# Optimization experiments

Hardware: AMD Instinct MI355X
Metric: run time of the kernel (lower is better)

## Reference

```python
import jax, jax.numpy as jnp
import numpy as np

N_NODES = 50000
N_EDGES = 400000
D_IN = 512
D_OUT = 512
MASK_RATE = 0.3


def setup_inputs() -> dict:
    key = jax.random.key(0)
    k1, k2, k3, k4, k5 = jax.random.split(key, 5)
    feat = jax.random.normal(k1, (N_NODES, D_IN), dtype=jnp.float32)
    # xavier_uniform for weight [in_feat, out_feat]
    limit = float(np.sqrt(6.0 / (D_IN + D_OUT)))
    weight = jax.random.uniform(k2, (D_IN, D_OUT), dtype=jnp.float32, minval=-limit, maxval=limit)
    edge_src = jax.random.randint(k3, (N_EDGES,), 0, N_NODES, dtype=jnp.int64 if jax.config.jax_enable_x64 else jnp.int32)
    edge_dst = jax.random.randint(k4, (N_EDGES,), 0, N_NODES, dtype=jnp.int64 if jax.config.jax_enable_x64 else jnp.int32)
    edge_val = jax.random.uniform(k5, (N_EDGES,), dtype=jnp.float32)
    # deterministic stand-in for torch.randperm(...)[:num_mask]
    perm = jax.random.permutation(jax.random.fold_in(key, 7), N_NODES)
    mask_idx = perm[: int(MASK_RATE * N_NODES)]
    return {
        "feat": feat,
        "weight": weight,
        "edge_val": edge_val,
        "edge_src": edge_src,
        "edge_dst": edge_dst,
        "mask_idx": mask_idx,
    }


def reference(feat, weight, edge_val, edge_src, edge_dst, mask_idx):
    # zero out masked node rows (encoding_mask_noise)
    out_x = feat.at[mask_idx].set(0.0)
    # dense transform: [N, D_in] @ [D_in, D_out]
    x = out_x @ weight
    # spmm(adj, x): for edge (src -> dst, val): out[dst] += val * x[src]
    msgs = edge_val[:, None] * x[edge_src]  # [E, D_out]
    out = jax.ops.segment_sum(msgs, edge_dst, num_segments=feat.shape[0])
    return out, mask_idx
```

## Files before the change

### kernel.cpp

```cpp
#include <hip/hip_runtime.h>

#define DD 512
#define SCAN_B 256
#define BM 128
#define BN 256
#define BK 32
#define NSTEP 16
typedef unsigned short u16;
typedef unsigned int u32;

typedef __attribute__((ext_vector_type(8))) __bf16 bf16v8;
typedef __attribute__((ext_vector_type(4))) float f32x4;

__device__ __forceinline__ u16 f2bf(float f) {
  u32 u = __builtin_bit_cast(u32, f);
  u32 r = (u + 0x7fffu + ((u >> 16) & 1u)) >> 16;
  return (u16)r;
}
__device__ __forceinline__ float bf2f(u32 h) {
  return __builtin_bit_cast(float, h << 16);
}
__device__ __forceinline__ u32 pk2(float a, float b) {
  return f2bf(a) | ((u32)f2bf(b) << 16);
}

typedef const __attribute__((address_space(1))) void* gptr_t;
typedef __attribute__((address_space(3))) void* lptr_t;
__device__ __forceinline__ void gload_lds16(const void* g, void* l) {
  __builtin_amdgcn_global_load_lds((gptr_t)g, (lptr_t)l, 16, 0, 0);
}

#define BAR_N(N)                                                        \
  do {                                                                  \
    __builtin_amdgcn_sched_barrier(0);                                  \
    asm volatile("s_waitcnt vmcnt(" #N ") lgkmcnt(0)\n\ts_barrier" ::: "memory"); \
  } while (0)

__global__ __launch_bounds__(256) void wconv_t(const float* __restrict__ W,
                                               u16* __restrict__ Wt) {
  __shared__ float sm[64][65];
  const int bx = blockIdx.x;
  const int by = blockIdx.y;
  const int t = threadIdx.x;
  const int r = t >> 6;
  const int c = t & 63;
#pragma unroll
  for (int i = 0; i < 64; i += 4)
    sm[i + r][c] = W[(size_t)(bx * 64 + i + r) * DD + by * 64 + c];
  __syncthreads();
#pragma unroll
  for (int i = 0; i < 64; i += 4) {
    const int n = by * 64 + i + r;
    const int k = bx * 64 + c;
    Wt[(size_t)n * DD + k] = f2bf(sm[c][i + r]);
  }
}

__global__ __launch_bounds__(512) void gemm_pipe(const float* __restrict__ A,
                                                 const u16* __restrict__ Bt,
                                                 u16* __restrict__ X, int M) {
  __shared__ __align__(16) u16 ldsA[2][BM * BK];
  __shared__ __align__(16) u16 ldsB[3][BN * BK];
  const int tid = threadIdx.x;
  const int lane = tid & 63;
  const int w = tid >> 6;
  const int wm = w >> 2;
  const int wn = w & 3;
  const int row0 = blockIdx.y * BM;
  const int colB = blockIdx.x * BN;
  const int lr = lane & 15;
  const int kg = lane >> 4;

  f32x4 acc[4][4] = {};

  const int arow = tid >> 2;
  const int agk = (tid & 3) ^ ((arow >> 1) & 3);
  int ar = row0 + arow;
  if (ar >= M) ar = M - 1;
  const float* gA = A + (size_t)ar * DD + agk * 8;
  const int laoff = tid * 8;

  const u16* gB[2];
  int lB[2];
#pragma unroll
  for (int q = 0; q < 2; ++q) {
    const int c = (w * 2 + q) * 64 + lane;
    const int col = c >> 2, kc = c & 3;
    const int gk = kc ^ ((col >> 1) & 3);
    gB[q] = Bt + (size_t)(colB + col) * DD + gk * 8;
    lB[q] = c * 8;
  }

  f32x4 rP[2][2];

#pragma unroll
  for (int q = 0; q < 2; ++q) gload_lds16(gB[q], &ldsB[0][lB[q]]);
#pragma unroll
  for (int q = 0; q < 2; ++q) gload_lds16(gB[q] + BK, &ldsB[1][lB[q]]);
  rP[0][0] = *(const f32x4*)(gA);
  rP[0][1] = *(const f32x4*)(gA + 4);
  rP[1][0] = *(const f32x4*)(gA + BK);
  rP[1][1] = *(const f32x4*)(gA + BK + 4);
  {
    uint4 pk;
    pk.x = pk2(rP[0][0].x, rP[0][0].y);
    pk.y = pk2(rP[0][0].z, rP[0][0].w);
    pk.z = pk2(rP[0][1].x, rP[0][1].y);
    pk.w = pk2(rP[0][1].z, rP[0][1].w);
    *(uint4*)&ldsA[0][laoff] = pk;
  }
  BAR_N(2);

#pragma unroll
  for (int t = 0; t < NSTEP; ++t) {
    if (t + 2 < NSTEP) {
#pragma unroll
      for (int q = 0; q < 2; ++q)
        gload_lds16(gB[q] + (t + 2) * BK, &ldsB[(t + 2) % 3][lB[q]]);
    }

    bf16v8 af[4], bfr[4];
#pragma unroll
    for (int m = 0; m < 4; ++m) {
      const int row = wm * 64 + m * 16 + lr;
      const int kc = kg ^ ((row >> 1) & 3);
      af[m] = *(const bf16v8*)&ldsA[t & 1][row * BK + kc * 8];
    }
#pragma unroll
    for (int n = 0; n < 4; ++n) {
      const int col = wn * 64 + n * 16 + lr;
      const int kc = kg ^ ((col >> 1) & 3);
      bfr[n] = *(const bf16v8*)&ldsB[t % 3][col * BK + kc * 8];
    }
#pragma unroll
    for (int m = 0; m < 4; ++m)
#pragma unroll
      for (int n = 0; n < 4; ++n)
        acc[m][n] = __builtin_amdgcn_mfma_f32_16x16x32_bf16(af[m], bfr[n], acc[m][n], 0, 0, 0);

    if (t + 1 < NSTEP) {
      uint4 pk;
      pk.x = pk2(rP[(t + 1) & 1][0].x, rP[(t + 1) & 1][0].y);
      pk.y = pk2(rP[(t + 1) & 1][0].z, rP[(t + 1) & 1][0].w);
      pk.z = pk2(rP[(t + 1) & 1][1].x, rP[(t + 1) & 1][1].y);
      pk.w = pk2(rP[(t + 1) & 1][1].z, rP[(t + 1) & 1][1].w);
      *(uint4*)&ldsA[(t + 1) & 1][laoff] = pk;
    }
    if (t + 2 < NSTEP) {
      rP[t & 1][0] = *(const f32x4*)(gA + (t + 2) * BK);
      rP[t & 1][1] = *(const f32x4*)(gA + (t + 2) * BK + 4);
    }

    if (t < NSTEP - 3)      BAR_N(4);
    else if (t < NSTEP - 1) BAR_N(0);
  }

  const int crow = (lane >> 4) * 4;
  const int ccol = lane & 15;
#pragma unroll
  for (int m = 0; m < 4; ++m) {
    const int rowb = row0 + wm * 64 + m * 16 + crow;
#pragma unroll
    for (int n = 0; n < 4; ++n) {
      const int col = colB + wn * 64 + n * 16 + ccol;
#pragma unroll
      for (int r = 0; r < 4; ++r)
        X[(size_t)(rowb + r) * DD + col] = f2bf(acc[m][n][r]);
    }
  }
}

__global__ void zero_rows(u16* __restrict__ x, const int* __restrict__ mask) {
  const int r = mask[blockIdx.x];
  *(uint4*)(x + (size_t)r * DD + threadIdx.x * 8) = make_uint4(0, 0, 0, 0);
}

__global__ __launch_bounds__(256) void hist(const int* __restrict__ dst,
                                            int* __restrict__ counts, int n) {
  const int i = blockIdx.x * blockDim.x + threadIdx.x;
  if (i < n) atomicAdd(&counts[dst[i]], 1);
}

__global__ __launch_bounds__(SCAN_B) void scanA(const int* __restrict__ counts,
                                                int* __restrict__ lscan,
                                                int* __restrict__ blockSums, int n) {
  __shared__ int sm[SCAN_B];
  const int t = threadIdx.x;
  const int i = blockIdx.x * SCAN_B + t;
  const int v = (i < n) ? counts[i] : 0;
  sm[t] = v;
  __syncthreads();
  for (int off = 1; off < SCAN_B; off <<= 1) {
    int add = (t >= off) ? sm[t - off] : 0;
    __syncthreads();
    sm[t] += add;
    __syncthreads();
  }
  if (i < n) lscan[i] = sm[t] - v;
  if (t == SCAN_B - 1) blockSums[blockIdx.x] = sm[t];
}

__global__ __launch_bounds__(SCAN_B) void scanB(int* __restrict__ blockSums, int nb) {
  __shared__ int sm[SCAN_B];
  const int t = threadIdx.x;
  const int v = (t < nb) ? blockSums[t] : 0;
  sm[t] = v;
  __syncthreads();
  for (int off = 1; off < SCAN_B; off <<= 1) {
    int add = (t >= off) ? sm[t - off] : 0;
    __syncthreads();
    sm[t] += add;
    __syncthreads();
  }
  if (t < nb) blockSums[t] = sm[t] - v;
}

__global__ __launch_bounds__(SCAN_B) void scanC(int* __restrict__ lscan,
                                                const int* __restrict__ blockBase,
                                                int* __restrict__ cursor, int n) {
  const int i = blockIdx.x * SCAN_B + threadIdx.x;
  if (i < n) {
    const int o = lscan[i] + blockBase[blockIdx.x];
    lscan[i] = o;
    cursor[i] = o;
  }
}

__global__ __launch_bounds__(256) void scatter_sort(const int* __restrict__ src,
                                                    const int* __restrict__ dst,
                                                    const float* __restrict__ ev,
                                                    int* __restrict__ cursor,
                                                    int* __restrict__ ssrc,
                                                    float* __restrict__ sval, int n) {
  const int i = blockIdx.x * blockDim.x + threadIdx.x;
  if (i < n) {
    const int pos = atomicAdd(&cursor[dst[i]], 1);
    ssrc[pos] = src[i];
    sval[pos] = ev[i];
  }
}

__global__ __launch_bounds__(256) void aggregate(const u16* __restrict__ x,
                                                 const int* __restrict__ ssrc,
                                                 const float* __restrict__ sval,
                                                 const int* __restrict__ offsets,
                                                 const int* __restrict__ counts,
                                                 float* __restrict__ out, int n_nodes) {
  const int node = blockIdx.x * 4 + (threadIdx.x >> 6);
  if (node >= n_nodes) return;
  const int lane = threadIdx.x & 63;
  const int b = offsets[node];
  const int cnt = counts[node];
  float acc[8] = {};
  for (int j = 0; j < cnt; ++j) {
    const int s = ssrc[b + j];
    const float v = sval[b + j];
    const uint4 u = *(const uint4*)(x + (size_t)s * DD + lane * 8);
    acc[0] = fmaf(v, bf2f(u.x & 0xffffu), acc[0]);
    acc[1] = fmaf(v, bf2f(u.x >> 16),     acc[1]);
    acc[2] = fmaf(v, bf2f(u.y & 0xffffu), acc[2]);
    acc[3] = fmaf(v, bf2f(u.y >> 16),     acc[3]);
    acc[4] = fmaf(v, bf2f(u.z & 0xffffu), acc[4]);
    acc[5] = fmaf(v, bf2f(u.z >> 16),     acc[5]);
    acc[6] = fmaf(v, bf2f(u.w & 0xffffu), acc[6]);
    acc[7] = fmaf(v, bf2f(u.w >> 16),     acc[7]);
  }
  f32x4* o = (f32x4*)(out + (size_t)node * DD + lane * 8);
  f32x4 o0 = {acc[0], acc[1], acc[2], acc[3]};
  f32x4 o1 = {acc[4], acc[5], acc[6], acc[7]};
  __builtin_nontemporal_store(o0, o);
  __builtin_nontemporal_store(o1, o + 1);
}

__global__ void mask_tail(const int* __restrict__ mask, float* __restrict__ out_tail,
                          int nm) {
  const int i = blockIdx.x * blockDim.x + threadIdx.x;
  if (i < nm) out_tail[i] = (float)mask[i];
}

extern "C" void kernel_launch(void* const* d_in, const int* in_sizes, int n_in,
                              void* d_out, int out_size, void* d_ws, size_t ws_size,
                              hipStream_t stream) {
  const float* feat     = (const float*)d_in[0];
  const float* weight   = (const float*)d_in[1];
  const float* edge_val = (const float*)d_in[2];
  const int*   edge_src = (const int*)d_in[3];
  const int*   edge_dst = (const int*)d_in[4];
  const int*   mask_idx = (const int*)d_in[5];

  const int n_nodes = in_sizes[0] / DD;
  const int n_edges = in_sizes[2];
  const int n_mask  = in_sizes[5];

  const int n_tiles_m = (n_nodes + BM - 1) / BM;
  const int m_pad = n_tiles_m * BM;

  float* out = (float*)d_out;

  char* base = (char*)d_ws;
  size_t off = 0;
  auto alloc = [&](size_t bytes) {
    void* p = base + off;
    off = (off + bytes + 255) & ~(size_t)255;
    return p;
  };
  u16*   x      = (u16*)alloc((size_t)m_pad * DD * sizeof(u16));
  u16*   wt     = (u16*)alloc((size_t)DD * DD * sizeof(u16));
  int*   counts = (int*)alloc((size_t)n_nodes * sizeof(int));
  int*   offs   = (int*)alloc((size_t)n_nodes * sizeof(int));
  int*   cursor = (int*)alloc((size_t)n_nodes * sizeof(int));
  int*   bsums  = (int*)alloc(SCAN_B * sizeof(int));
  int*   ssrc   = (int*)alloc((size_t)n_edges * sizeof(int));
  float* sval   = (float*)alloc((size_t)n_edges * sizeof(float));

  const int nb = (n_nodes + SCAN_B - 1) / SCAN_B;

  (void)hipMemsetAsync(counts, 0, (size_t)n_nodes * sizeof(int), stream);
  hist<<<(n_edges + 255) / 256, 256, 0, stream>>>(edge_dst, counts, n_edges);
  scanA<<<nb, SCAN_B, 0, stream>>>(counts, offs, bsums, n_nodes);
  scanB<<<1, SCAN_B, 0, stream>>>(bsums, nb);
  scanC<<<nb, SCAN_B, 0, stream>>>(offs, bsums, cursor, n_nodes);
  scatter_sort<<<(n_edges + 255) / 256, 256, 0, stream>>>(edge_src, edge_dst, edge_val,
                                                          cursor, ssrc, sval, n_edges);

  dim3 wg(DD / 64, DD / 64);
  wconv_t<<<wg, 256, 0, stream>>>(weight, wt);
  dim3 grid(DD / BN, n_tiles_m);
  gemm_pipe<<<grid, 512, 0, stream>>>(feat, wt, x, n_nodes);
  zero_rows<<<n_mask, 64, 0, stream>>>(x, mask_idx);

  aggregate<<<(n_nodes + 3) / 4, 256, 0, stream>>>(x, ssrc, sval, offs, counts, out, n_nodes);

  mask_tail<<<(n_mask + 255) / 256, 256, 0, stream>>>(mask_idx, out + (size_t)n_nodes * DD, n_mask);
}
```

Measured before the change: 190.4 us.

## Deepen GEMM A-prefetch, unroll aggregation gathers, and fuse small launch kernels

The GEMM now prefetches A tiles three steps ahead instead of two, adjusts the vmcnt waits to match, adds a second sched_barrier after each barrier, and sets a launch-bounds occupancy hint. The aggregation loop is unrolled by four so several row gathers are in flight at once. The scanB kernel is folded into scanC by having every block redo the small block-sum scan, and mask_tail is merged into the row-zeroing kernel, removing two launches. Costs are higher register pressure in the GEMM and aggregate kernels and redundant scan work in each scanC block.

Result: slower. 239.0 us (+25.5%).

```diff
diff --git a/kernel.cpp b/kernel.cpp
--- a/kernel.cpp
+++ b/kernel.cpp
@@ -34,6 +34,7 @@
   do {                                                                  \
     __builtin_amdgcn_sched_barrier(0);                                  \
     asm volatile("s_waitcnt vmcnt(" #N ") lgkmcnt(0)\n\ts_barrier" ::: "memory"); \
+    __builtin_amdgcn_sched_barrier(0);                                  \
   } while (0)
 
 __global__ __launch_bounds__(256) void wconv_t(const float* __restrict__ W,
@@ -56,9 +57,9 @@
   }
 }
 
-__global__ __launch_bounds__(512) void gemm_pipe(const float* __restrict__ A,
-                                                 const u16* __restrict__ Bt,
-                                                 u16* __restrict__ X, int M) {
+__global__ __launch_bounds__(512, 4) void gemm_pipe(const float* __restrict__ A,
+                                                    const u16* __restrict__ Bt,
+                                                    u16* __restrict__ X, int M) {
   __shared__ __align__(16) u16 ldsA[2][BM * BK];
   __shared__ __align__(16) u16 ldsB[3][BN * BK];
   const int tid = threadIdx.x;
@@ -91,16 +92,17 @@
     lB[q] = c * 8;
   }
 
-  f32x4 rP[2][2];
+  f32x4 rP[3][2];
 
 #pragma unroll
   for (int q = 0; q < 2; ++q) gload_lds16(gB[q], &ldsB[0][lB[q]]);
 #pragma unroll
   for (int q = 0; q < 2; ++q) gload_lds16(gB[q] + BK, &ldsB[1][lB[q]]);
-  rP[0][0] = *(const f32x4*)(gA);
-  rP[0][1] = *(const f32x4*)(gA + 4);
-  rP[1][0] = *(const f32x4*)(gA + BK);
-  rP[1][1] = *(const f32x4*)(gA + BK + 4);
+#pragma unroll
+  for (int p = 0; p < 3; ++p) {
+    rP[p][0] = *(const f32x4*)(gA + p * BK);
+    rP[p][1] = *(const f32x4*)(gA + p * BK + 4);
+  }
   {
     uint4 pk;
     pk.x = pk2(rP[0][0].x, rP[0][0].y);
@@ -109,7 +111,7 @@
     pk.w = pk2(rP[0][1].z, rP[0][1].w);
     *(uint4*)&ldsA[0][laoff] = pk;
   }
-  BAR_N(2);
+  BAR_N(4);
 
 #pragma unroll
   for (int t = 0; t < NSTEP; ++t) {
@@ -139,19 +141,21 @@
         acc[m][n] = __builtin_amdgcn_mfma_f32_16x16x32_bf16(af[m], bfr[n], acc[m][n], 0, 0, 0);
 
     if (t + 1 < NSTEP) {
+      const f32x4 p0 = rP[(t + 1) % 3][0];
+      const f32x4 p1 = rP[(t + 1) % 3][1];
       uint4 pk;
-      pk.x = pk2(rP[(t + 1) & 1][0].x, rP[(t + 1) & 1][0].y);
-      pk.y = pk2(rP[(t + 1) & 1][0].z, rP[(t + 1) & 1][0].w);
-      pk.z = pk2(rP[(t + 1) & 1][1].x, rP[(t + 1) & 1][1].y);
-      pk.w = pk2(rP[(t + 1) & 1][1].z, rP[(t + 1) & 1][1].w);
+      pk.x = pk2(p0.x, p0.y);
+      pk.y = pk2(p0.z, p0.w);
+      pk.z = pk2(p1.x, p1.y);
+      pk.w = pk2(p1.z, p1.w);
       *(uint4*)&ldsA[(t + 1) & 1][laoff] = pk;
     }
-    if (t + 2 < NSTEP) {
-      rP[t & 1][0] = *(const f32x4*)(gA + (t + 2) * BK);
-      rP[t & 1][1] = *(const f32x4*)(gA + (t + 2) * BK + 4);
-    }
-
-    if (t < NSTEP - 3)      BAR_N(4);
+    if (t + 3 < NSTEP) {
+      rP[(t + 3) % 3][0] = *(const f32x4*)(gA + (t + 3) * BK);
+      rP[(t + 3) % 3][1] = *(const f32x4*)(gA + (t + 3) * BK + 4);
+    }
+
+    if (t < NSTEP - 3)      BAR_N(6);
     else if (t < NSTEP - 1) BAR_N(0);
   }
 
@@ -170,8 +174,11 @@
   }
 }
 
-__global__ void zero_rows(u16* __restrict__ x, const int* __restrict__ mask) {
-  const int r = mask[blockIdx.x];
+__global__ void zero_mask(u16* __restrict__ x, const int* __restrict__ mask,
+                          float* __restrict__ out_tail) {
+  const int b = blockIdx.x;
+  const int r = mask[b];
+  if (threadIdx.x == 0) out_tail[b] = (float)r;
   *(uint4*)(x + (size_t)r * DD + threadIdx.x * 8) = make_uint4(0, 0, 0, 0);
 }
 
@@ -200,7 +207,9 @@
   if (t == SCAN_B - 1) blockSums[blockIdx.x] = sm[t];
 }
 
-__global__ __launch_bounds__(SCAN_B) void scanB(int* __restrict__ blockSums, int nb) {
+__global__ __launch_bounds__(SCAN_B) void scanC(int* __restrict__ lscan,
+                                                const int* __restrict__ blockSums,
+                                                int* __restrict__ cursor, int n, int nb) {
   __shared__ int sm[SCAN_B];
   const int t = threadIdx.x;
   const int v = (t < nb) ? blockSums[t] : 0;
@@ -212,15 +221,10 @@
     sm[t] += add;
     __syncthreads();
   }
-  if (t < nb) blockSums[t] = sm[t] - v;
-}
-
-__global__ __launch_bounds__(SCAN_B) void scanC(int* __restrict__ lscan,
-                                                const int* __restrict__ blockBase,
-                                                int* __restrict__ cursor, int n) {
-  const int i = blockIdx.x * SCAN_B + threadIdx.x;
+  const int base = sm[blockIdx.x] - ((blockIdx.x < nb) ? blockSums[blockIdx.x] : 0);
+  const int i = blockIdx.x * SCAN_B + t;
   if (i < n) {
-    const int o = lscan[i] + blockBase[blockIdx.x];
+    const int o = lscan[i] + base;
     lscan[i] = o;
     cursor[i] = o;
   }
@@ -250,32 +254,41 @@
   if (node >= n_nodes) return;
   const int lane = threadIdx.x & 63;
   const int b = offsets[node];
-  const int cnt = counts[node];
+  const int e = b + counts[node];
   float acc[8] = {};
-  for (int j = 0; j < cnt; ++j) {
-    const int s = ssrc[b + j];
-    const float v = sval[b + j];
+  int j = b;
+#define AGG1(U, V)                                      \
+  do {                                                  \
+    acc[0] = fmaf(V, bf2f(U.x & 0xffffu), acc[0]);      \
+    acc[1] = fmaf(V, bf2f(U.x >> 16),     acc[1]);      \
+    acc[2] = fmaf(V, bf2f(U.y & 0xffffu), acc[2]);      \
+    acc[3] = fmaf(V, bf2f(U.y >> 16),     acc[3]);      \
+    acc[4] = fmaf(V, bf2f(U.z & 0xffffu), acc[4]);      \
+    acc[5] = fmaf(V, bf2f(U.z >> 16),     acc[5]);      \
+    acc[6] = fmaf(V, bf2f(U.w & 0xffffu), acc[6]);      \
+    acc[7] = fmaf(V, bf2f(U.w >> 16),     acc[7]);      \
+  } while (0)
+  for (; j + 4 <= e; j += 4) {
+    const int s0 = ssrc[j], s1 = ssrc[j + 1], s2 = ssrc[j + 2], s3 = ssrc[j + 3];
+    const float v0 = sval[j], v1 = sval[j + 1], v2 = sval[j + 2], v3 = sval[j + 3];
+    const uint4 u0 = *(const uint4*)(x + (size_t)s0 * DD + lane * 8);
+    const uint4 u1 = *(const uint4*)(x + (size_t)s1 * DD + lane * 8);
+    const uint4 u2 = *(const uint4*)(x + (size_t)s2 * DD + lane * 8);
+    const uint4 u3 = *(const uint4*)(x + (size_t)s3 * DD + lane * 8);
+    AGG1(u0, v0); AGG1(u1, v1); AGG1(u2, v2); AGG1(u3, v3);
+  }
+  for (; j < e; ++j) {
+    const int s = ssrc[j];
+    const float v = sval[j];
     const uint4 u = *(const uint4*)(x + (size_t)s * DD + lane * 8);
-    acc[0] = fmaf(v, bf2f(u.x & 0xffffu), acc[0]);
-    acc[1] = fmaf(v, bf2f(u.x >> 16),     acc[1]);
-    acc[2] = fmaf(v, bf2f(u.y & 0xffffu), acc[2]);
-    acc[3] = fmaf(v, bf2f(u.y >> 16),     acc[3]);
-    acc[4] = fmaf(v, bf2f(u.z & 0xffffu), acc[4]);
-    acc[5] = fmaf(v, bf2f(u.z >> 16),     acc[5]);
-    acc[6] = fmaf(v, bf2f(u.w & 0xffffu), acc[6]);
-    acc[7] = fmaf(v, bf2f(u.w >> 16),     acc[7]);
-  }
+    AGG1(u, v);
+  }
+#undef AGG1
   f32x4* o = (f32x4*)(out + (size_t)node * DD + lane * 8);
   f32x4 o0 = {acc[0], acc[1], acc[2], acc[3]};
   f32x4 o1 = {acc[4], acc[5], acc[6], acc[7]};
   __builtin_nontemporal_store(o0, o);
   __builtin_nontemporal_store(o1, o + 1);
-}
-
-__global__ void mask_tail(const int* __restrict__ mask, float* __restrict__ out_tail,
-                          int nm) {
-  const int i = blockIdx.x * blockDim.x + threadIdx.x;
-  if (i < nm) out_tail[i] = (float)mask[i];
 }
 
 extern "C" void kernel_launch(void* const* d_in, const int* in_sizes, int n_in,
@@ -318,8 +331,7 @@
   (void)hipMemsetAsync(counts, 0, (size_t)n_nodes * sizeof(int), stream);
   hist<<<(n_edges + 255) / 256, 256, 0, stream>>>(edge_dst, counts, n_edges);
   scanA<<<nb, SCAN_B, 0, stream>>>(counts, offs, bsums, n_nodes);
-  scanB<<<1, SCAN_B, 0, stream>>>(bsums, nb);
-  scanC<<<nb, SCAN_B, 0, stream>>>(offs, bsums, cursor, n_nodes);
+  scanC<<<nb, SCAN_B, 0, stream>>>(offs, bsums, cursor, n_nodes, nb);
   scatter_sort<<<(n_edges + 255) / 256, 256, 0, stream>>>(edge_src, edge_dst, edge_val,
                                                           cursor, ssrc, sval, n_edges);
 
@@ -327,9 +339,7 @@
   wconv_t<<<wg, 256, 0, stream>>>(weight, wt);
   dim3 grid(DD / BN, n_tiles_m);
   gemm_pipe<<<grid, 512, 0, stream>>>(feat, wt, x, n_nodes);
-  zero_rows<<<n_mask, 64, 0, stream>>>(x, mask_idx);
+  zero_mask<<<n_mask, 64, 0, stream>>>(x, mask_idx, out + (size_t)n_nodes * DD);
 
   aggregate<<<(n_nodes + 3) / 4, 256, 0, stream>>>(x, ssrc, sval, offs, counts, out, n_nodes);
-
-  mask_tail<<<(n_mask + 255) / 256, 256, 0, stream>>>(mask_idx, out + (size_t)n_nodes * DD, n_mask);
-}
+}
```
